# Optimization experiments

Measured on AMD Instinct MI355X. Metric: run time of the kernel, lower is better.

Reference implementation:

```python
import jax, jax.numpy as jnp
import numpy as np

D = 1e-6
B, N, E, K = 128, 512, 512, 256


def _lower_median_abs(x, axis):
    # torch.median returns the LOWER of the two middle values for even counts
    n = x.shape[axis]
    s = jnp.sort(jnp.abs(x), axis=axis)
    return jnp.take(s, (n - 1) // 2, axis=axis)


def _bounds_from_cauchy(head, errors, k):
    # errors: (B, E, *head.shape[1:]); E divisible by k in this config
    b, e = errors.shape[0], errors.shape[1]
    tail = errors.shape[2:]
    chunks = errors.reshape(b, e // k, k, *tail)
    l1 = _lower_median_abs(chunks, axis=2).sum(axis=1)
    return head - l1, head + l1


def _relaxed_exp(h, errs, noise, lb, ub):
    is_tight = ub == lb
    lam_s = (jnp.exp(ub) - jnp.exp(lb)) / (ub - lb + D)
    lam = jnp.minimum(lam_s, jnp.exp(lb + 1.0 - 0.1))
    ub0 = jnp.where(lam > lam_s, jnp.exp(lb) - lam * lb, jnp.exp(ub) - lam * ub)
    mu = 0.5 * (lam * (1.0 - jnp.log(lam)) + ub0)
    delta = 0.5 * (ub0 - lam * (1.0 - jnp.log(lam)))
    lam = jnp.where(is_tight, 0.0, lam)
    mu = jnp.where(is_tight, jnp.exp(ub), mu)
    delta = jnp.where(is_tight, 0.0, delta)
    new_head = h * lam + mu
    new_errs = jnp.concatenate([errs * lam[:, None], delta[:, None] * noise], axis=1)
    return new_head, new_errs


def _relaxed_log(h, errs, noise, lb, ub):
    is_tight = ub == lb
    lam_s = (jnp.log(ub) - jnp.log(lb + D)) / (ub - lb + D)
    lam = lam_s
    lb0 = jnp.where(lam < lam_s, jnp.log(ub) - ub * lam, jnp.log(lb + D) - lb * lam)
    mu = 0.5 * (-jnp.log(lam) - 1.0 + lb0)
    delta = 0.5 * (-jnp.log(lam) - 1.0 - lb0)
    lam = jnp.where(is_tight, 0.0, lam)
    mu = jnp.where(is_tight, jnp.log(ub), mu)
    delta = jnp.where(is_tight, 0.0, delta)
    new_head = h * lam + mu
    new_errs = jnp.concatenate([errs * lam[:, None], delta[:, None] * noise], axis=1)
    return new_head, new_errs


def setup_inputs() -> dict:
    key = jax.random.key(0)
    k1, k2, k3, k4 = jax.random.split(key, 4)
    curr_head = jax.random.normal(k1, (B, N), dtype=jnp.float32)
    # small error magnitudes keep exp/log relaxation bounds valid (lb of log stage > 0)
    curr_errors = 1e-3 * jax.random.normal(k2, (B * E, N), dtype=jnp.float32)
    cauchy_exp = jax.random.cauchy(k3, (B, K, N), dtype=jnp.float32)
    cauchy_log = jax.random.cauchy(k4, (B, K), dtype=jnp.float32)
    return {"curr_head": curr_head, "curr_errors": curr_errors,
            "cauchy_exp": cauchy_exp, "cauchy_log": cauchy_log, "k": K}


def reference(curr_head, curr_errors, cauchy_exp, cauchy_log, k):
    b, n = curr_head.shape
    max_head = jax.lax.stop_gradient(jnp.max(curr_head, axis=1, keepdims=True))  # (B,1)
    temp_head = curr_head - max_head                         # (B,N)
    errs = curr_errors.reshape(b, -1, n)                     # (B,E,N)
    lb, ub = _bounds_from_cauchy(temp_head, errs, k)
    exp_head, exp_errs = _relaxed_exp(temp_head, errs, cauchy_exp, lb, ub)  # (B,N),(B,E+K,N)
    exp_head = exp_head.sum(axis=1)                          # (B,)
    exp_errs = exp_errs.sum(axis=2)                          # (B,E+K)
    lb2, ub2 = _bounds_from_cauchy(exp_head, exp_errs, k)
    ls_head, ls_errs = _relaxed_log(exp_head, exp_errs, cauchy_log, lb2, ub2)  # (B,),(B,E+2K)
    ls_head = ls_head + max_head[:, 0]
    return ls_head, ls_errs.reshape(-1)
```

## Files before the change

### kernel.cpp

```cpp
#include <hip/hip_runtime.h>
#include <cstdint>
#include <cstddef>

#define BB 128
#define NN 512
#define EE 512
#define KK 256
#define STR 17

__device__ __forceinline__ float wave_reduce_max(float v) {
#pragma unroll
  for (int off = 32; off >= 1; off >>= 1) v = fmaxf(v, __shfl_xor(v, off, 64));
  return v;
}
__device__ __forceinline__ float wave_reduce_sum(float v) {
#pragma unroll
  for (int off = 32; off >= 1; off >>= 1) v += __shfl_xor(v, off, 64);
  return v;
}

template <int CTRL>
__device__ __forceinline__ float dppz(float x) {
  return __int_as_float(__builtin_amdgcn_update_dpp(0, __float_as_int(x), CTRL, 0xf, 0xf, false));
}
template <int CTRL>
__device__ __forceinline__ float dppi(float x) {
  return __int_as_float(__builtin_amdgcn_update_dpp(__float_as_int(x), __float_as_int(x), CTRL, 0xf, 0xf, false));
}
__device__ __forceinline__ float wave_sum64(float x) {
  x += dppz<0x111>(x); x += dppz<0x112>(x); x += dppz<0x114>(x); x += dppz<0x118>(x);
  x += dppz<0x142>(x); x += dppz<0x143>(x);
  return __int_as_float(__builtin_amdgcn_readlane(__float_as_int(x), 63));
}
__device__ __forceinline__ float wave_max64nn(float x) {
  x = fmaxf(x, dppz<0x111>(x)); x = fmaxf(x, dppz<0x112>(x));
  x = fmaxf(x, dppz<0x114>(x)); x = fmaxf(x, dppz<0x118>(x));
  x = fmaxf(x, dppz<0x142>(x)); x = fmaxf(x, dppz<0x143>(x));
  return __int_as_float(__builtin_amdgcn_readlane(__float_as_int(x), 63));
}
__device__ __forceinline__ float wave_min64(float x) {
  x = fminf(x, dppi<0x111>(x)); x = fminf(x, dppi<0x112>(x));
  x = fminf(x, dppi<0x114>(x)); x = fminf(x, dppi<0x118>(x));
  x = fminf(x, dppi<0x142>(x)); x = fminf(x, dppi<0x143>(x));
  return __int_as_float(__builtin_amdgcn_readlane(__float_as_int(x), 63));
}

__device__ __forceinline__ float wave_median256_fast(float a0, float a1, float a2, float a3) {
  float S = wave_sum64((a0 + a1) + (a2 + a3));
  float mean = S * 0.00390625f;
  float lo = 0.f, hi = S * 1.0000002f + 1e-37f;
  int c_lo = 0, c_hi = 256;
  float piv = 0.845f * mean;
  float ans = 0.f;
  bool have = false;
#pragma unroll 1
  for (int it = 0; it < 34; ++it) {
    if (!(piv > lo && piv < hi)) piv = 0.5f * (lo + hi);
    int cnt = __popcll(__ballot(a0 < piv)) + __popcll(__ballot(a1 < piv)) +
              __popcll(__ballot(a2 < piv)) + __popcll(__ballot(a3 < piv));
    if (cnt == 128) {
      float m = fmaxf(fmaxf(a0 < piv ? a0 : 0.f, a1 < piv ? a1 : 0.f),
                      fmaxf(a2 < piv ? a2 : 0.f, a3 < piv ? a3 : 0.f));
      ans = wave_max64nn(m); have = true; break;
    }
    if (cnt == 127) {
      float m = fminf(fminf(a0 >= piv ? a0 : 3.4e38f, a1 >= piv ? a1 : 3.4e38f),
                      fminf(a2 >= piv ? a2 : 3.4e38f, a3 >= piv ? a3 : 3.4e38f));
      ans = wave_min64(m); have = true; break;
    }
    if (cnt < 127) { lo = piv; c_lo = cnt; } else { hi = piv; c_hi = cnt; }
    if (it == 0) piv = piv + (127.5f - (float)cnt) * mean * 0.0077f;
    else piv = lo + (hi - lo) * ((127.5f - (float)c_lo) / (float)(c_hi - c_lo));
    if (it >= 10) piv = 0.5f * (lo + hi);
  }
  if (!have) {
    float m = fmaxf(fmaxf(a0 < hi ? a0 : 0.f, a1 < hi ? a1 : 0.f),
                    fmaxf(a2 < hi ? a2 : 0.f, a3 < hi ? a3 : 0.f));
    ans = wave_max64nn(m);
  }
  return ans;
}

__global__ __launch_bounds__(256, 4) void kfused(
    const float* __restrict__ head, const float* __restrict__ errs,
    float* __restrict__ ws_delta, float* __restrict__ ws_htpart,
    float* __restrict__ ws_epart) {
  __shared__ float tile[512 * STR];
  __shared__ float medbuf[32];
  __shared__ float lambuf[16];
  __shared__ float redm[4];
  const int blk = blockIdx.x;
  const int b = blk >> 5, g = blk & 31;
  const int n0 = g * 16;
  const int tid = threadIdx.x, wave = tid >> 6, lane = tid & 63;

  float m = fmaxf(head[(size_t)b * NN + tid], head[(size_t)b * NN + 256 + tid]);
  m = wave_reduce_max(m);
  if (lane == 0) redm[wave] = m;

  const int tr = tid >> 2, tc = (tid & 3) * 4;
  const float* src = errs + (size_t)b * EE * NN + n0 + tc;
#pragma unroll
  for (int i = 0; i < 8; ++i) {
    int row = i * 64 + tr;
    float4 v = *(const float4*)(src + (size_t)row * NN);
    float* dst = &tile[row * STR + tc];
    dst[0] = v.x; dst[1] = v.y; dst[2] = v.z; dst[3] = v.w;
  }
  __syncthreads();
  float hmax = fmaxf(fmaxf(redm[0], redm[1]), fmaxf(redm[2], redm[3]));

#pragma unroll 1
  for (int j = 0; j < 8; ++j) {
    int p = wave * 8 + j;
    int col = p & 15;
    int rb = (p >> 4) * 256;
    float a0 = fabsf(tile[(rb + lane) * STR + col]);
    float a1 = fabsf(tile[(rb + lane + 64) * STR + col]);
    float a2 = fabsf(tile[(rb + lane + 128) * STR + col]);
    float a3 = fabsf(tile[(rb + lane + 192) * STR + col]);
    float med = wave_median256_fast(a0, a1, a2, a3);
    if (lane == 0) medbuf[p] = med;
  }
  __syncthreads();

  float htp = 0.f;
  if (tid < 16) {
    int n = n0 + tid;
    float l1 = medbuf[tid] + medbuf[16 + tid];
    float th = head[(size_t)b * NN + n] - hmax;
    float lb = th - l1, ub = th + l1;
    float lam, mu, delta;
    if (ub == lb) {
      lam = 0.f; mu = expf(ub); delta = 0.f;
    } else {
      float elb = expf(lb), eub = expf(ub);
      float lam_s = (eub - elb) / (ub - lb + 1e-6f);
      lam = fminf(lam_s, expf(lb + 0.9f));
      float ub0 = (lam > lam_s) ? (elb - lam * lb) : (eub - lam * ub);
      float t = lam * (1.f - logf(lam));
      mu = 0.5f * (t + ub0);
      delta = 0.5f * (ub0 - t);
    }
    lambuf[tid] = lam;
    ws_delta[(size_t)b * NN + n] = delta;
    htp = th * lam + mu;
  }
  if (wave == 0) {
    float s = wave_reduce_sum(htp);
    if (lane == 0) ws_htpart[b * 32 + g] = s;
  }
  __syncthreads();

  float s0 = 0.f, s1 = 0.f;
#pragma unroll
  for (int j = 0; j < 16; ++j) {
    float w = lambuf[j];
    s0 = fmaf(tile[tid * STR + j], w, s0);
    s1 = fmaf(tile[(tid + 256) * STR + j], w, s1);
  }
  float* op = ws_epart + ((size_t)(b * 32 + g)) * 512;
  op[tid] = s0;
  op[tid + 256] = s1;
}

__global__ __launch_bounds__(256) void kcexp(
    const float* __restrict__ cexp, const float* __restrict__ ws_delta,
    float* __restrict__ ws_ee2) {
  const int blk = blockIdx.x;
  const int b = blk >> 2, part = blk & 3;
  const int wave = threadIdx.x >> 6, lane = threadIdx.x & 63;
  const float* wsrc = ws_delta + (size_t)b * NN;
  float4 wa = *(const float4*)(wsrc + 4 * lane);
  float4 wb = *(const float4*)(wsrc + 256 + 4 * lane);
  const int r0 = part * 64 + wave * 16;
  const float* base = cexp + (size_t)b * KK * NN;
  float* out = ws_ee2 + (size_t)b * KK;
#pragma unroll 1
  for (int i = 0; i < 16; ++i) {
    int r = r0 + i;
    const float* rp = base + (size_t)r * NN;
    float4 x = *(const float4*)(rp + 4 * lane);
    float4 y = *(const float4*)(rp + 256 + 4 * lane);
    float s = x.x * wa.x + x.y * wa.y + x.z * wa.z + x.w * wa.w +
              y.x * wb.x + y.y * wb.y + y.z * wb.z + y.w * wb.w;
    s = wave_reduce_sum(s);
    if (lane == 0) out[r] = s;
  }
}

__global__ __launch_bounds__(256) void kstage3(
    const float* __restrict__ head, const float* __restrict__ clog,
    const float* __restrict__ ws_htpart, const float* __restrict__ ws_epart,
    const float* __restrict__ ws_ee2, float* __restrict__ out) {
  __shared__ float eb[768];
  __shared__ float redm[4];
  __shared__ float meds[3];
  __shared__ float sc[2];
  __shared__ float ehsh;
  const int b = blockIdx.x;
  const int tid = threadIdx.x, wave = tid >> 6, lane = tid & 63;

  float m = fmaxf(head[(size_t)b * NN + tid], head[(size_t)b * NN + 256 + tid]);
  m = wave_reduce_max(m);
  if (lane == 0) redm[wave] = m;

  float acc0 = 0.f, acc1 = 0.f;
  const float* pp = ws_epart + (size_t)b * 32 * 512;
#pragma unroll
  for (int g = 0; g < 32; ++g) {
    acc0 += pp[g * 512 + tid];
    acc1 += pp[g * 512 + 256 + tid];
  }
  eb[tid] = acc0;
  eb[tid + 256] = acc1;
  eb[tid + 512] = ws_ee2[(size_t)b * KK + tid];
  __syncthreads();

  if (wave < 3) {
    const float* p = eb + wave * 256;
    float a0 = fabsf(p[lane]), a1 = fabsf(p[lane + 64]);
    float a2 = fabsf(p[lane + 128]), a3 = fabsf(p[lane + 192]);
    float med = wave_median256_fast(a0, a1, a2, a3);
    if (lane == 0) meds[wave] = med;
  } else {
    float v = (lane < 32) ? ws_htpart[b * 32 + lane] : 0.f;
    v = wave_reduce_sum(v);
    if (lane == 0) ehsh = v;
  }
  __syncthreads();

  if (tid == 0) {
    float hmax = fmaxf(fmaxf(redm[0], redm[1]), fmaxf(redm[2], redm[3]));
    float eh = ehsh;
    float l1 = meds[0] + meds[1] + meds[2];
    float lb = eh - l1, ub = eh + l1;
    float lam, mu, delta;
    if (ub == lb) {
      lam = 0.f; mu = logf(ub); delta = 0.f;
    } else {
      float llb = logf(lb + 1e-6f);
      float lam_s = (logf(ub) - llb) / (ub - lb + 1e-6f);
      lam = lam_s;
      float lb0 = llb - lb * lam;
      float t = -logf(lam) - 1.f;
      mu = 0.5f * (t + lb0);
      delta = 0.5f * (t - lb0);
    }
    sc[0] = lam; sc[1] = delta;
    out[b] = eh * lam + mu + hmax;
  }
  __syncthreads();
  float lam = sc[0], delta = sc[1];
  float* ob = out + BB + (size_t)b * 1024;
  ob[tid] = eb[tid] * lam;
  ob[tid + 256] = eb[tid + 256] * lam;
  ob[tid + 512] = eb[tid + 512] * lam;
  ob[tid + 768] = delta * clog[(size_t)b * KK + tid];
}

extern "C" void kernel_launch(void* const* d_in, const int* in_sizes, int n_in,
                              void* d_out, int out_size, void* d_ws, size_t ws_size,
                              hipStream_t stream) {
  const float* head = (const float*)d_in[0];
  const float* errs = (const float*)d_in[1];
  const float* cexp = (const float*)d_in[2];
  const float* clog = (const float*)d_in[3];
  float* out = (float*)d_out;

  float* ws = (float*)d_ws;
  float* ws_delta = ws;
  float* ws_htpart = ws_delta + BB * NN;
  float* ws_ee2 = ws_htpart + BB * 32;
  float* ws_epart = ws_ee2 + BB * KK;

  hipLaunchKernelGGL(kfused, dim3(BB * 32), dim3(256), 0, stream,
                     head, errs, ws_delta, ws_htpart, ws_epart);
  hipLaunchKernelGGL(kcexp, dim3(BB * 4), dim3(256), 0, stream,
                     cexp, ws_delta, ws_ee2);
  hipLaunchKernelGGL(kstage3, dim3(BB), dim3(256), 0, stream,
                     head, clog, ws_htpart, ws_epart, ws_ee2, out);
}
```

Measured before the change: 270.4 us.

## Fuse cauchy_exp contraction into main fused kernel, drop separate kcexp launch

The main kernel now prefetches its 16-column slice of cauchy_exp into registers while the error tile loads. After computing lambda, it reuses the shared tile to contract that slice with delta, writing per-group partial sums. This removes the separate kcexp launch and the delta workspace round trip. In exchange it adds register pressure and an extra partial-sum array of 32 per batch row that kstage3 must read and reduce.

Measured after the change: 270.7 us. No clear change (+0.1%).

```diff
diff --git a/kernel.cpp b/kernel.cpp
--- a/kernel.cpp
+++ b/kernel.cpp
@@ -83,22 +83,23 @@
 
 __global__ __launch_bounds__(256, 4) void kfused(
     const float* __restrict__ head, const float* __restrict__ errs,
-    float* __restrict__ ws_delta, float* __restrict__ ws_htpart,
-    float* __restrict__ ws_epart) {
+    const float* __restrict__ cexp, float* __restrict__ ws_htpart,
+    float* __restrict__ ws_epart, float* __restrict__ ws_cpart) {
   __shared__ float tile[512 * STR];
   __shared__ float medbuf[32];
   __shared__ float lambuf[16];
+  __shared__ float deltabuf[16];
   __shared__ float redm[4];
   const int blk = blockIdx.x;
   const int b = blk >> 5, g = blk & 31;
   const int n0 = g * 16;
   const int tid = threadIdx.x, wave = tid >> 6, lane = tid & 63;
+  const int tr = tid >> 2, tc = (tid & 3) * 4;
 
   float m = fmaxf(head[(size_t)b * NN + tid], head[(size_t)b * NN + 256 + tid]);
   m = wave_reduce_max(m);
   if (lane == 0) redm[wave] = m;
 
-  const int tr = tid >> 2, tc = (tid & 3) * 4;
   const float* src = errs + (size_t)b * EE * NN + n0 + tc;
 #pragma unroll
   for (int i = 0; i < 8; ++i) {
@@ -107,6 +108,11 @@
     float* dst = &tile[row * STR + tc];
     dst[0] = v.x; dst[1] = v.y; dst[2] = v.z; dst[3] = v.w;
   }
+  const float* csrc = cexp + (size_t)b * KK * NN + n0 + tc;
+  float4 c4[4];
+#pragma unroll
+  for (int i = 0; i < 4; ++i) c4[i] = *(const float4*)(csrc + (size_t)(i * 64 + tr) * NN);
+
   __syncthreads();
   float hmax = fmaxf(fmaxf(redm[0], redm[1]), fmaxf(redm[2], redm[3]));
 
@@ -143,7 +149,7 @@
       delta = 0.5f * (ub0 - t);
     }
     lambuf[tid] = lam;
-    ws_delta[(size_t)b * NN + n] = delta;
+    deltabuf[tid] = delta;
     htp = th * lam + mu;
   }
   if (wave == 0) {
@@ -162,37 +168,24 @@
   float* op = ws_epart + ((size_t)(b * 32 + g)) * 512;
   op[tid] = s0;
   op[tid + 256] = s1;
-}
-
-__global__ __launch_bounds__(256) void kcexp(
-    const float* __restrict__ cexp, const float* __restrict__ ws_delta,
-    float* __restrict__ ws_ee2) {
-  const int blk = blockIdx.x;
-  const int b = blk >> 2, part = blk & 3;
-  const int wave = threadIdx.x >> 6, lane = threadIdx.x & 63;
-  const float* wsrc = ws_delta + (size_t)b * NN;
-  float4 wa = *(const float4*)(wsrc + 4 * lane);
-  float4 wb = *(const float4*)(wsrc + 256 + 4 * lane);
-  const int r0 = part * 64 + wave * 16;
-  const float* base = cexp + (size_t)b * KK * NN;
-  float* out = ws_ee2 + (size_t)b * KK;
-#pragma unroll 1
-  for (int i = 0; i < 16; ++i) {
-    int r = r0 + i;
-    const float* rp = base + (size_t)r * NN;
-    float4 x = *(const float4*)(rp + 4 * lane);
-    float4 y = *(const float4*)(rp + 256 + 4 * lane);
-    float s = x.x * wa.x + x.y * wa.y + x.z * wa.z + x.w * wa.w +
-              y.x * wb.x + y.y * wb.y + y.z * wb.z + y.w * wb.w;
-    s = wave_reduce_sum(s);
-    if (lane == 0) out[r] = s;
-  }
+  __syncthreads();
+
+#pragma unroll
+  for (int i = 0; i < 4; ++i) {
+    float* dst = &tile[(i * 64 + tr) * STR + tc];
+    dst[0] = c4[i].x; dst[1] = c4[i].y; dst[2] = c4[i].z; dst[3] = c4[i].w;
+  }
+  __syncthreads();
+  float cs = 0.f;
+#pragma unroll
+  for (int j = 0; j < 16; ++j) cs = fmaf(tile[tid * STR + j], deltabuf[j], cs);
+  ws_cpart[((size_t)(b * 32 + g)) * 256 + tid] = cs;
 }
 
 __global__ __launch_bounds__(256) void kstage3(
     const float* __restrict__ head, const float* __restrict__ clog,
     const float* __restrict__ ws_htpart, const float* __restrict__ ws_epart,
-    const float* __restrict__ ws_ee2, float* __restrict__ out) {
+    const float* __restrict__ ws_cpart, float* __restrict__ out) {
   __shared__ float eb[768];
   __shared__ float redm[4];
   __shared__ float meds[3];
@@ -205,16 +198,18 @@
   m = wave_reduce_max(m);
   if (lane == 0) redm[wave] = m;
 
-  float acc0 = 0.f, acc1 = 0.f;
+  float acc0 = 0.f, acc1 = 0.f, acc2 = 0.f;
   const float* pp = ws_epart + (size_t)b * 32 * 512;
+  const float* cp = ws_cpart + (size_t)b * 32 * 256;
 #pragma unroll
   for (int g = 0; g < 32; ++g) {
     acc0 += pp[g * 512 + tid];
     acc1 += pp[g * 512 + 256 + tid];
+    acc2 += cp[g * 256 + tid];
   }
   eb[tid] = acc0;
   eb[tid + 256] = acc1;
-  eb[tid + 512] = ws_ee2[(size_t)b * KK + tid];
+  eb[tid + 512] = acc2;
   __syncthreads();
 
   if (wave < 3) {
@@ -269,15 +264,12 @@
   float* out = (float*)d_out;
 
   float* ws = (float*)d_ws;
-  float* ws_delta = ws;
-  float* ws_htpart = ws_delta + BB * NN;
-  float* ws_ee2 = ws_htpart + BB * 32;
-  float* ws_epart = ws_ee2 + BB * KK;
+  float* ws_htpart = ws;
+  float* ws_epart = ws_htpart + BB * 32;
+  float* ws_cpart = ws_epart + BB * 32 * 512;
 
   hipLaunchKernelGGL(kfused, dim3(BB * 32), dim3(256), 0, stream,
-                     head, errs, ws_delta, ws_htpart, ws_epart);
-  hipLaunchKernelGGL(kcexp, dim3(BB * 4), dim3(256), 0, stream,
-                     cexp, ws_delta, ws_ee2);
+                     head, errs, cexp, ws_htpart, ws_epart, ws_cpart);
   hipLaunchKernelGGL(kstage3, dim3(BB), dim3(256), 0, stream,
-                     head, clog, ws_htpart, ws_epart, ws_ee2, out);
-}
+                     head, clog, ws_htpart, ws_epart, ws_cpart, out);
+}
```
